# Performance work log

Hardware: AMD Instinct MI355X
Metric: run time of the kernel (lower is better)

## Reference

```python
import jax, jax.numpy as jnp
import numpy as np

T, B, N = 2048, 32, 1024   # time, batch, dan_hidden_size
H = 8                      # multihead_size
N2 = 128                   # attention_hidden_size
K = N // H                 # N_H = 128 per-head dim
K2 = N2 // H               # N2_H = 16 per-head attention dim


def setup_inputs() -> dict:
    key = jax.random.key(0)
    ks = jax.random.split(key, 10)
    s_n = 1.0 / np.sqrt(N)
    s_k = 1.0 / np.sqrt(K)
    s_k2 = 1.0 / np.sqrt(K2)
    return {
        "hyp": jax.random.normal(ks[0], (T, B, N), dtype=jnp.float32),
        # H independent per-head linears N -> K, stacked: (H, K, N)
        "Wmh": jax.random.uniform(ks[1], (H, K, N), minval=-s_n, maxval=s_n, dtype=jnp.float32),
        "bmh": jax.random.uniform(ks[2], (H, K), minval=-s_n, maxval=s_n, dtype=jnp.float32),
        # shared W: K -> K2
        "W": jax.random.uniform(ks[3], (K2, K), minval=-s_k, maxval=s_k, dtype=jnp.float32),
        "bW": jax.random.uniform(ks[4], (K2,), minval=-s_k, maxval=s_k, dtype=jnp.float32),
        # shared W_m: K -> K2
        "Wm": jax.random.uniform(ks[5], (K2, K), minval=-s_k, maxval=s_k, dtype=jnp.float32),
        "bWm": jax.random.uniform(ks[6], (K2,), minval=-s_k, maxval=s_k, dtype=jnp.float32),
        # shared W_h: K2 -> 1
        "Wh": jax.random.uniform(ks[7], (K2,), minval=-s_k2, maxval=s_k2, dtype=jnp.float32),
        "bWh": jax.random.uniform(ks[8], (), minval=-s_k2, maxval=s_k2, dtype=jnp.float32),
        "dan_hidden_size": N,
        "attention_hidden_size": N2,
        "multihead_size": H,
    }


def reference(hyp, Wmh, bmh, W, bW, Wm, bWm, Wh, bWh,
              dan_hidden_size, attention_hidden_size, multihead_size):
    # Per-head projections, all heads at once: (B, T, H, K)
    X = jnp.einsum('tbn,hkn->bthk', hyp, Wmh) + bmh
    # mean over time (original x.mean(0)): (B, H, K)
    m = X.mean(axis=1)
    # tanh-gated additive scoring: (B, T, H, K2)
    g = jnp.tanh(jnp.einsum('bthk,qk->bthq', X, W) + bW) \
        * jnp.tanh(jnp.einsum('bhk,qk->bhq', m, Wm) + bWm)[:, None]
    # scalar score per (b, t, h), softmax over time
    s = jnp.einsum('bthq,q->bth', g, Wh) + bWh
    a = jax.nn.softmax(s, axis=1)                       # (B, T, H)
    # attention-weighted sum over time: (B, H, K)
    c = jnp.einsum('bth,bthk->bhk', a, X)
    # concat heads along feature dim (head-major order, matches torch.cat)
    Bsz = c.shape[0]
    return c.reshape(Bsz, -1)                            # (B, N)
```

## Files before the change

### kernel.cpp

```cpp
#include <hip/hip_runtime.h>
#include <hip/hip_bf16.h>

#define T_DIM 2048
#define B_DIM 32
#define N_DIM 1024
#define H_DIM 8
#define K_DIM 128
#define Q_DIM 16

typedef __bf16 bf16x8 __attribute__((ext_vector_type(8)));
typedef __bf16 bf16x4 __attribute__((ext_vector_type(4)));
typedef float  f32x4  __attribute__((ext_vector_type(4)));

__device__ inline bf16x8 cvt8(float4 a, float4 b) {
    bf16x8 r;
    r[0] = (__bf16)a.x; r[1] = (__bf16)a.y; r[2] = (__bf16)a.z; r[3] = (__bf16)a.w;
    r[4] = (__bf16)b.x; r[5] = (__bf16)b.y; r[6] = (__bf16)b.z; r[7] = (__bf16)b.w;
    return r;
}

__global__ __launch_bounds__(256)
void cvt_f32_bf16(const float* __restrict__ s, __bf16* __restrict__ d)
{
    const long i = ((long)blockIdx.x * 256 + threadIdx.x) * 8;
    float4 a = *(const float4*)(s + i);
    float4 b = *(const float4*)(s + i + 4);
    *(bf16x8*)(d + i) = cvt8(a, b);
}

__global__ __launch_bounds__(512, 1)
void gemm_x_8ph(const __bf16* __restrict__ A, const __bf16* __restrict__ Bw,
                const float* __restrict__ bias, __bf16* __restrict__ X,
                float* __restrict__ mpart)
{
    __shared__ __bf16 ldsA[2][16384];
    __shared__ __bf16 ldsB[2][16384];
    __bf16* ldsAf = &ldsA[0][0];
    __bf16* ldsBf = &ldsB[0][0];

    const int tid  = threadIdx.x;
    const int lane = tid & 63;
    const int w    = tid >> 6;
    const int wm   = w >> 2;
    const int wn   = w & 3;

    const int bid  = blockIdx.x;
    const int wgid = (bid & 7) * 128 + (bid >> 3);
    const int bm   = wgid >> 2;
    const int bn   = wgid & 3;
    const long row0 = (long)bm * 256;
    const long col0 = (long)bn * 256;

    const int srow = w * 8 + (lane >> 3);
    const int scol = ((lane & 7) ^ (lane >> 3)) * 8;
    const __bf16* Ag = A  + (row0 + srow) * 1024 + scol;
    const __bf16* Bg = Bw + (col0 + srow) * 1024 + scol;
    const int ldst = w * 512;

    const int fr = lane & 15;
    const int g2 = lane >> 4;
    const int x7 = lane & 7;

    const __bf16* aK0 = ldsAf + (wm * 128 + fr) * 64 + ((g2    ) ^ x7) * 8;
    const __bf16* aK1 = ldsAf + (wm * 128 + fr) * 64 + ((4 + g2) ^ x7) * 8;
    const __bf16* bK0 = ldsBf + (wn * 64  + fr) * 64 + ((g2    ) ^ x7) * 8;
    const __bf16* bK1 = ldsBf + (wn * 64  + fr) * 64 + ((4 + g2) ^ x7) * 8;

    f32x4 acc[8][4];
    #pragma unroll
    for (int i = 0; i < 8; ++i)
        #pragma unroll
        for (int j = 0; j < 4; ++j)
            acc[i][j] = f32x4{0.f, 0.f, 0.f, 0.f};

    #define GLDA(SRC_, DST_) __builtin_amdgcn_global_load_lds( \
        (const __attribute__((address_space(1))) void*)(SRC_), \
        (__attribute__((address_space(3))) void*)(DST_), 16, 0, 0)

    #pragma unroll
    for (int j = 0; j < 2; ++j) GLDA(Ag + (long)j * 65536,          ldsAf + j * 4096 + ldst);
    #pragma unroll
    for (int j = 0; j < 2; ++j) GLDA(Ag + 131072 + (long)j * 65536, ldsAf + 8192 + j * 4096 + ldst);
    #pragma unroll
    for (int j = 0; j < 2; ++j) GLDA(Bg + (long)j * 65536,          ldsBf + j * 4096 + ldst);
    #pragma unroll
    for (int j = 0; j < 2; ++j) GLDA(Bg + 131072 + (long)j * 65536, ldsBf + 8192 + j * 4096 + ldst);
    #pragma unroll
    for (int j = 0; j < 2; ++j) GLDA(Bg + 64 + (long)j * 65536,          ldsBf + 16384 + j * 4096 + ldst);
    #pragma unroll
    for (int j = 0; j < 2; ++j) GLDA(Bg + 64 + 131072 + (long)j * 65536, ldsBf + 16384 + 8192 + j * 4096 + ldst);
    asm volatile("s_waitcnt vmcnt(4)" ::: "memory");
    __builtin_amdgcn_sched_barrier(0);
    __builtin_amdgcn_s_barrier();

    const __bf16* AgN = Ag + 64;
    const __bf16* BgN = Bg + 128;

    #define MFMA16(AF_, BF_, OFF_)                                             \
        __builtin_amdgcn_s_setprio(1);                                         \
        _Pragma("unroll") for (int mi = 0; mi < 4; ++mi)                       \
            _Pragma("unroll") for (int ni = 0; ni < 4; ++ni)                   \
                acc[mi + (OFF_)][ni] = __builtin_amdgcn_mfma_f32_16x16x32_bf16(\
                    BF_[ni], AF_[mi], acc[mi + (OFF_)][ni], 0, 0, 0);          \
        __builtin_amdgcn_s_setprio(0);

    #define LGKM0()                                                            \
        asm volatile("s_waitcnt lgkmcnt(0)" ::: "memory");                     \
        __builtin_amdgcn_sched_barrier(0);

    #define KTBODY(SO_, SN_, KO_, STGA_, STGB_, VM_)                           \
    {                                                                          \
        bf16x8 a0[4], b0[4], a0h[4], b1[4], a1[4], a1h[4];                     \
        _Pragma("unroll") for (int mi = 0; mi < 4; ++mi)                       \
            a0[mi] = *(const bf16x8*)(aK0 + (SO_) + mi * 1024);                \
        _Pragma("unroll") for (int ni = 0; ni < 4; ++ni)                       \
            b0[ni] = *(const bf16x8*)(bK0 + (SO_) + ni * 1024);                \
        if (STGA_) {                                                           \
            _Pragma("unroll") for (int j = 0; j < 2; ++j)                      \
                GLDA(AgN + (KO_) + (long)j * 65536,                            \
                     ldsAf + (SN_) + j * 4096 + ldst);                         \
        }                                                                      \
        __builtin_amdgcn_s_barrier();                                          \
        LGKM0();                                                               \
        MFMA16(a0, b0, 0);                                                     \
        __builtin_amdgcn_s_barrier();                                          \
        _Pragma("unroll") for (int mi = 0; mi < 4; ++mi)                       \
            a0h[mi] = *(const bf16x8*)(aK1 + (SO_) + mi * 1024);               \
        _Pragma("unroll") for (int ni = 0; ni < 4; ++ni)                       \
            b1[ni]  = *(const bf16x8*)(bK1 + (SO_) + ni * 1024);               \
        if (STGA_) {                                                           \
            _Pragma("unroll") for (int j = 0; j < 2; ++j)                      \
                GLDA(AgN + (KO_) + 131072 + (long)j * 65536,                   \
                     ldsAf + (SN_) + 8192 + j * 4096 + ldst);                  \
        }                                                                      \
        __builtin_amdgcn_s_barrier();                                          \
        LGKM0();                                                               \
        MFMA16(a0h, b1, 0);                                                    \
        __builtin_amdgcn_s_barrier();                                          \
        _Pragma("unroll") for (int mi = 0; mi < 4; ++mi)                       \
            a1[mi] = *(const bf16x8*)(aK0 + (SO_) + (mi + 4) * 1024);          \
        if (STGB_) {                                                           \
            _Pragma("unroll") for (int j = 0; j < 2; ++j)                      \
                GLDA(BgN + (KO_) + (long)j * 65536,                            \
                     ldsBf + (SO_) + j * 4096 + ldst);                         \
        }                                                                      \
        __builtin_amdgcn_s_barrier();                                          \
        LGKM0();                                                               \
        MFMA16(a1, b0, 4);                                                     \
        __builtin_amdgcn_s_barrier();                                          \
        _Pragma("unroll") for (int mi = 0; mi < 4; ++mi)                       \
            a1h[mi] = *(const bf16x8*)(aK1 + (SO_) + (mi + 4) * 1024);         \
        if (STGB_) {                                                           \
            _Pragma("unroll") for (int j = 0; j < 2; ++j)                      \
                GLDA(BgN + (KO_) + 131072 + (long)j * 65536,                   \
                     ldsBf + (SO_) + 8192 + j * 4096 + ldst);                  \
        }                                                                      \
        if ((VM_) == 4)      { asm volatile("s_waitcnt vmcnt(4)" ::: "memory"); } \
        else if ((VM_) == 0) { asm volatile("s_waitcnt vmcnt(0)" ::: "memory"); } \
        __builtin_amdgcn_sched_barrier(0);                                     \
        __builtin_amdgcn_s_barrier();                                          \
        LGKM0();                                                               \
        MFMA16(a1h, b1, 4);                                                    \
        __builtin_amdgcn_s_barrier();                                          \
    }

    #pragma unroll 1
    for (int ii = 0; ii < 7; ++ii) {
        KTBODY(0,     16384, 0,  1, 1, 4);
        KTBODY(16384, 0,     64, 1, 1, 4);
        AgN += 128; BgN += 128;
    }
    KTBODY(0,     16384, 0, 1, 0, 0);
    KTBODY(16384, 0,     0, 0, 0, -1);
    #undef KTBODY
    #undef MFMA16
    #undef LGKM0
    #undef GLDA

    const int g4 = lane >> 4;
    const long colb = col0 + wn * 64 + g4 * 4;

    float4 bias4[4];
    #pragma unroll
    for (int ni = 0; ni < 4; ++ni)
        bias4[ni] = *(const float4*)(bias + colb + ni * 16);

    f32x4 msum[2][4];
    #pragma unroll
    for (int bh = 0; bh < 2; ++bh)
        #pragma unroll
        for (int ni = 0; ni < 4; ++ni)
            msum[bh][ni] = f32x4{0.f, 0.f, 0.f, 0.f};

    #pragma unroll
    for (int mi = 0; mi < 8; ++mi) {
        const long row = row0 + wm * 128 + mi * 16 + fr;
        #pragma unroll
        for (int ni = 0; ni < 4; ++ni) {
            f32x4 xv;
            xv[0] = acc[mi][ni][0] + bias4[ni].x;
            xv[1] = acc[mi][ni][1] + bias4[ni].y;
            xv[2] = acc[mi][ni][2] + bias4[ni].z;
            xv[3] = acc[mi][ni][3] + bias4[ni].w;
            bf16x4 xb;
            xb[0] = (__bf16)xv[0]; xb[1] = (__bf16)xv[1];
            xb[2] = (__bf16)xv[2]; xb[3] = (__bf16)xv[3];
            *(bf16x4*)(X + row * 1024 + colb + ni * 16) = xb;
            msum[mi & 1][ni] += xv;
        }
    }

    float* ldsf = (float*)ldsAf;
    __syncthreads();
    if (wm == 1) {
        #pragma unroll
        for (int bh = 0; bh < 2; ++bh)
            #pragma unroll
            for (int ni = 0; ni < 4; ++ni)
                *(f32x4*)(ldsf + (bh * 16 + fr) * 256 + wn * 64 + ni * 16 + g4 * 4) = msum[bh][ni];
    }
    __syncthreads();
    if (wm == 0) {
        #pragma unroll
        for (int bh = 0; bh < 2; ++bh) {
            const int b = bh * 16 + fr;
            #pragma unroll
            for (int ni = 0; ni < 4; ++ni) {
                f32x4 other = *(const f32x4*)(ldsf + b * 256 + wn * 64 + ni * 16 + g4 * 4);
                f32x4 tot = msum[bh][ni] + other;
                *(f32x4*)(mpart + ((long)bm * 32 + b) * 1024 + colb + ni * 16) = tot;
            }
        }
    }
}

__global__ __launch_bounds__(256)
void gate2_k(const float* __restrict__ mpart, const float* __restrict__ Wm,
             const float* __restrict__ bWm, float* __restrict__ g2)
{
    __shared__ float mrow[1024];
    const int b = blockIdx.x;
    const int j4 = threadIdx.x * 4;
    f32x4 s = f32x4{0.f, 0.f, 0.f, 0.f};
    for (int bm = 0; bm < 256; ++bm)
        s += *(const f32x4*)(mpart + ((long)bm * 32 + b) * 1024 + j4);
    mrow[j4 + 0] = s[0] * (1.0f / 2048.0f);
    mrow[j4 + 1] = s[1] * (1.0f / 2048.0f);
    mrow[j4 + 2] = s[2] * (1.0f / 2048.0f);
    mrow[j4 + 3] = s[3] * (1.0f / 2048.0f);
    __syncthreads();
    if (threadIdx.x < 128) {
        const int h = threadIdx.x >> 4;
        const int q = threadIdx.x & 15;
        float d = bWm[q];
        #pragma unroll 8
        for (int k = 0; k < 128; ++k) d += mrow[h * 128 + k] * Wm[q * 128 + k];
        g2[(b * 8 + h) * 16 + q] = tanhf(d);
    }
}

__global__ __launch_bounds__(256)
void attn_k(const __bf16* __restrict__ X, const float* __restrict__ W,
            const float* __restrict__ bW, const float* __restrict__ g2,
            const float* __restrict__ Wh, float* __restrict__ out)
{
    __shared__ float sch[64];
    __shared__ float pl[64];
    __shared__ float red[1024];
    __shared__ float scal[3];

    const int tid  = threadIdx.x;
    const int lane = tid & 63;
    const int w    = tid >> 6;
    const int bh   = blockIdx.x;
    const int b    = bh >> 3;
    const int h    = bh & 7;
    const int q    = lane & 15;
    const int g4   = lane >> 4;

    if (tid == 0) { scal[0] = -1e30f; scal[1] = 0.f; scal[2] = 0.f; }

    bf16x8 bfr[4];
    #pragma unroll
    for (int c = 0; c < 4; ++c) {
        const float* wp = W + q * 128 + c * 32 + g4 * 8;
        float4 w0 = *(const float4*)wp;
        float4 w1 = *(const float4*)(wp + 4);
        bfr[c] = cvt8(w0, w1);
    }
    const float whq = Wh[q];
    const float bWv = bW[q];
    const float gq  = g2[(b * 8 + h) * 16 + q];

    const __bf16* xp = X + ((long)(w * 16 + q) * 32 + b) * 1024 + h * 128 + g4 * 8;
    const int tr = tid >> 5;
    const int kq = tid & 31;
    const __bf16* xa = X + ((long)tr * 32 + b) * 1024 + h * 128 + kq * 4;

    float c0 = 0.f, c1 = 0.f, c2 = 0.f, c3 = 0.f;

    __syncthreads();

    #pragma unroll 1
    for (int ch = 0; ch < 32; ++ch) {
        bf16x8 afr[4];
        #pragma unroll
        for (int c = 0; c < 4; ++c) afr[c] = *(const bf16x8*)(xp + c * 32);
        f32x4 acc = f32x4{0.f, 0.f, 0.f, 0.f};
        #pragma unroll
        for (int c = 0; c < 4; ++c)
            acc = __builtin_amdgcn_mfma_f32_16x16x32_bf16(afr[c], bfr[c], acc, 0, 0, 0);
        #pragma unroll
        for (int r = 0; r < 4; ++r) {
            float val = tanhf(acc[r] + bWv) * gq * whq;
            val += __shfl_xor(val, 1);
            val += __shfl_xor(val, 2);
            val += __shfl_xor(val, 4);
            val += __shfl_xor(val, 8);
            if (q == 0) sch[w * 16 + g4 * 4 + r] = val;
        }
        __syncthreads();

        if (tid < 64) {
            float v = sch[tid];
            float mx = v;
            #pragma unroll
            for (int off = 1; off < 64; off <<= 1)
                mx = fmaxf(mx, __shfl_xor(mx, off));
            const float mold = scal[0];
            const float newm = fmaxf(mold, mx);
            const float f    = __expf(mold - newm);
            const float p    = __expf(v - newm);
            pl[tid] = p;
            float ps = p;
            #pragma unroll
            for (int off = 1; off < 64; off <<= 1)
                ps += __shfl_xor(ps, off);
            if (tid == 0) {
                scal[0] = newm;
                scal[1] = f;
                scal[2] = scal[2] * f + ps;
            }
        }
        __syncthreads();

        const float f = scal[1];
        if (f != 1.0f) { c0 *= f; c1 *= f; c2 *= f; c3 *= f; }
        #pragma unroll
        for (int i = 0; i < 8; ++i) {
            const float p = pl[tr + 8 * i];
            bf16x4 xv = *(const bf16x4*)(xa + (long)(8 * i) * 32768);
            c0 += p * (float)xv[0];
            c1 += p * (float)xv[1];
            c2 += p * (float)xv[2];
            c3 += p * (float)xv[3];
        }
        __syncthreads();

        xp += 64 * 32768;
        xa += 64 * 32768;
    }

    red[tr * 128 + kq * 4 + 0] = c0;
    red[tr * 128 + kq * 4 + 1] = c1;
    red[tr * 128 + kq * 4 + 2] = c2;
    red[tr * 128 + kq * 4 + 3] = c3;
    __syncthreads();
    if (tid < 128) {
        float s = 0.f;
        #pragma unroll
        for (int r = 0; r < 8; ++r) s += red[r * 128 + tid];
        out[b * 1024 + h * 128 + tid] = s / scal[2];
    }
}

extern "C" void kernel_launch(void* const* d_in, const int* in_sizes, int n_in,
                              void* d_out, int out_size, void* d_ws, size_t ws_size,
                              hipStream_t stream)
{
    const float* hyp = (const float*)d_in[0];
    const float* Wmh = (const float*)d_in[1];
    const float* bmh = (const float*)d_in[2];
    const float* W   = (const float*)d_in[3];
    const float* bW  = (const float*)d_in[4];
    const float* Wm  = (const float*)d_in[5];
    const float* bWm = (const float*)d_in[6];
    const float* Wh  = (const float*)d_in[7];
    float* out = (float*)d_out;

    char* ws = (char*)d_ws;
    const size_t SZ_X   = 134217728;
    const size_t SZ_AB  = 134217728;
    const size_t SZ_BB  = 2097152;
    const size_t SZ_MP  = 33554432;
    const size_t SZ_G2  = 16384;

    size_t off = 0;
    __bf16* X     = (__bf16*)(ws + off); off += SZ_X;
    __bf16* Ab    = (__bf16*)(ws + off); off += SZ_AB;
    __bf16* Bb    = (__bf16*)(ws + off); off += SZ_BB;
    float*  mpart = (float*) (ws + off); off += SZ_MP;
    float*  g2    = (float*) (ws + off); off += SZ_G2;

    cvt_f32_bf16<<<32768, 256, 0, stream>>>(hyp, Ab);
    cvt_f32_bf16<<<512,   256, 0, stream>>>(Wmh, Bb);
    gemm_x_8ph<<<1024, 512, 0, stream>>>(Ab, Bb, bmh, X, mpart);
    gate2_k<<<32, 256, 0, stream>>>(mpart, Wm, bWm, g2);
    attn_k<<<256, 256, 0, stream>>>(X, W, bW, g2, Wh, out);
}
```

Measured before the change: 340.0 us.

## Split attention softmax over time chunks with a separate merge kernel

The attention kernel previously ran one block per (batch, head) and walked all 2048 timesteps serially, which gave only 256 blocks. It now splits time into 8 chunks of 256, giving 2048 blocks that each write a partial weighted sum plus their running max and sum. A new merge kernel rescales the partials flash-decoding style to form the final softmax-weighted output. The aim is to fill the GPU better during the attention phase, at the cost of an extra launch and a small partial-result buffer.

```diff
diff --git a/kernel.cpp b/kernel.cpp
--- a/kernel.cpp
+++ b/kernel.cpp
@@ -260,9 +260,10 @@
 }
 
 __global__ __launch_bounds__(256)
-void attn_k(const __bf16* __restrict__ X, const float* __restrict__ W,
-            const float* __restrict__ bW, const float* __restrict__ g2,
-            const float* __restrict__ Wh, float* __restrict__ out)
+void attn_part(const __bf16* __restrict__ X, const float* __restrict__ W,
+               const float* __restrict__ bW, const float* __restrict__ g2,
+               const float* __restrict__ Wh,
+               float* __restrict__ partC, float* __restrict__ partML)
 {
     __shared__ float sch[64];
     __shared__ float pl[64];
@@ -272,7 +273,9 @@
     const int tid  = threadIdx.x;
     const int lane = tid & 63;
     const int w    = tid >> 6;
-    const int bh   = blockIdx.x;
+    const int bx   = blockIdx.x;
+    const int bh   = bx & 255;
+    const int tc   = bx >> 8;
     const int b    = bh >> 3;
     const int h    = bh & 7;
     const int q    = lane & 15;
@@ -292,17 +295,18 @@
     const float bWv = bW[q];
     const float gq  = g2[(b * 8 + h) * 16 + q];
 
-    const __bf16* xp = X + ((long)(w * 16 + q) * 32 + b) * 1024 + h * 128 + g4 * 8;
+    const long t0 = (long)tc * 256;
+    const __bf16* xp = X + ((t0 + w * 16 + q) * 32 + b) * 1024 + h * 128 + g4 * 8;
     const int tr = tid >> 5;
     const int kq = tid & 31;
-    const __bf16* xa = X + ((long)tr * 32 + b) * 1024 + h * 128 + kq * 4;
+    const __bf16* xa = X + ((t0 + tr) * 32 + b) * 1024 + h * 128 + kq * 4;
 
     float c0 = 0.f, c1 = 0.f, c2 = 0.f, c3 = 0.f;
 
     __syncthreads();
 
     #pragma unroll 1
-    for (int ch = 0; ch < 32; ++ch) {
+    for (int ch = 0; ch < 4; ++ch) {
         bf16x8 afr[4];
         #pragma unroll
         for (int c = 0; c < 4; ++c) afr[c] = *(const bf16x8*)(xp + c * 32);
@@ -370,8 +374,43 @@
         float s = 0.f;
         #pragma unroll
         for (int r = 0; r < 8; ++r) s += red[r * 128 + tid];
-        out[b * 1024 + h * 128 + tid] = s / scal[2];
-    }
+        partC[((long)bh * 8 + tc) * 128 + tid] = s;
+    }
+    if (tid == 0) {
+        partML[(bh * 8 + tc) * 2 + 0] = scal[0];
+        partML[(bh * 8 + tc) * 2 + 1] = scal[2];
+    }
+}
+
+__global__ __launch_bounds__(128)
+void attn_merge(const float* __restrict__ partC, const float* __restrict__ partML,
+                float* __restrict__ out)
+{
+    __shared__ float wgt[8];
+    __shared__ float lsum;
+    const int bh = blockIdx.x;
+    const int k  = threadIdx.x;
+    if (k == 0) {
+        float m = -1e30f;
+        #pragma unroll
+        for (int tc = 0; tc < 8; ++tc) m = fmaxf(m, partML[(bh * 8 + tc) * 2]);
+        float l = 0.f;
+        #pragma unroll
+        for (int tc = 0; tc < 8; ++tc) {
+            float e = __expf(partML[(bh * 8 + tc) * 2] - m);
+            wgt[tc] = e;
+            l += partML[(bh * 8 + tc) * 2 + 1] * e;
+        }
+        lsum = l;
+    }
+    __syncthreads();
+    float s = 0.f;
+    #pragma unroll
+    for (int tc = 0; tc < 8; ++tc)
+        s += partC[((long)bh * 8 + tc) * 128 + k] * wgt[tc];
+    const int b = bh >> 3;
+    const int h = bh & 7;
+    out[b * 1024 + h * 128 + k] = s / lsum;
 }
 
 extern "C" void kernel_launch(void* const* d_in, const int* in_sizes, int n_in,
@@ -394,17 +433,22 @@
     const size_t SZ_BB  = 2097152;
     const size_t SZ_MP  = 33554432;
     const size_t SZ_G2  = 16384;
+    const size_t SZ_PC  = 1048576;
+    const size_t SZ_PM  = 16384;
 
     size_t off = 0;
-    __bf16* X     = (__bf16*)(ws + off); off += SZ_X;
-    __bf16* Ab    = (__bf16*)(ws + off); off += SZ_AB;
-    __bf16* Bb    = (__bf16*)(ws + off); off += SZ_BB;
-    float*  mpart = (float*) (ws + off); off += SZ_MP;
-    float*  g2    = (float*) (ws + off); off += SZ_G2;
+    __bf16* X      = (__bf16*)(ws + off); off += SZ_X;
+    __bf16* Ab     = (__bf16*)(ws + off); off += SZ_AB;
+    __bf16* Bb     = (__bf16*)(ws + off); off += SZ_BB;
+    float*  mpart  = (float*) (ws + off); off += SZ_MP;
+    float*  g2     = (float*) (ws + off); off += SZ_G2;
+    float*  partC  = (float*) (ws + off); off += SZ_PC;
+    float*  partML = (float*) (ws + off); off += SZ_PM;
 
     cvt_f32_bf16<<<32768, 256, 0, stream>>>(hyp, Ab);
     cvt_f32_bf16<<<512,   256, 0, stream>>>(Wmh, Bb);
     gemm_x_8ph<<<1024, 512, 0, stream>>>(Ab, Bb, bmh, X, mpart);
     gate2_k<<<32, 256, 0, stream>>>(mpart, Wm, bWm, g2);
-    attn_k<<<256, 256, 0, stream>>>(X, W, bW, g2, Wh, out);
-}
+    attn_part<<<2048, 256, 0, stream>>>(X, W, bW, g2, Wh, partC, partML);
+    attn_merge<<<256, 128, 0, stream>>>(partC, partML, out);
+}
```

Result: faster. 298.8 us (-12.1%).
